# Kernel tuning notes

Hardware: AMD Instinct MI355X
Metric: run time of the kernel (lower is better)

## Reference

```python
import jax, jax.numpy as jnp
import numpy as np

B, L, D, H, NL = 4, 2048, 128, 4, 2
DH = D // H
FF = 2 * D
EPS_LN = 1e-5


def _p(key, shape, scale=0.05):
    return (jax.random.normal(key, shape, dtype=jnp.float32) * scale)


def setup_inputs() -> dict:
    key = jax.random.key(0)
    ks = jax.random.split(key, 40)
    inp = {
        "local_global": jax.random.normal(ks[0], (B, D), dtype=jnp.float32),
        "task_features": jax.random.normal(ks[1], (B, L, 15), dtype=jnp.float32),
        "privacy_features": jax.random.normal(ks[2], (B, L, 6), dtype=jnp.float32),
        "dag_features": jax.random.normal(ks[3], (B, L, 4), dtype=jnp.float32),
        # float mask in [0,1); values > 0.5 are MASKED (set to -inf) per torch code
        "attn_mask": jax.random.uniform(ks[4], (B, L, L), dtype=jnp.float32),
        # input projections (stored [in, out]; torch Linear does x @ W.T + b)
        "task_W": _p(ks[5], (15, D)), "task_b": jnp.zeros((D,), jnp.float32),
        "priv_W": _p(ks[6], (6, D)), "priv_b": jnp.zeros((D,), jnp.float32),
        "dag_W": _p(ks[7], (4, D)), "dag_b": jnp.zeros((D,), jnp.float32),
        "pre_g": jnp.ones((D,), jnp.float32), "pre_b": jnp.zeros((D,), jnp.float32),
        "post_g": jnp.ones((D,), jnp.float32), "post_b": jnp.zeros((D,), jnp.float32),
        "out_W": _p(ks[8], (D, D)), "out_b": jnp.zeros((D,), jnp.float32),
        # per-layer params stacked on leading NL axis
        "qW": _p(ks[9], (NL, D, D)), "qb": jnp.zeros((NL, D), jnp.float32),
        "kW": _p(ks[10], (NL, D, D)), "kb": jnp.zeros((NL, D), jnp.float32),
        "vW": _p(ks[11], (NL, D, D)), "vb": jnp.zeros((NL, D), jnp.float32),
        "oW": _p(ks[12], (NL, D, D)), "ob": jnp.zeros((NL, D), jnp.float32),
        "n1g": jnp.ones((NL, D), jnp.float32), "n1b": jnp.zeros((NL, D), jnp.float32),
        "n2g": jnp.ones((NL, D), jnp.float32), "n2b": jnp.zeros((NL, D), jnp.float32),
        "f1W": _p(ks[13], (NL, D, FF)), "f1b": jnp.zeros((NL, FF), jnp.float32),
        "f2W": _p(ks[14], (NL, FF, D)), "f2b": jnp.zeros((NL, D), jnp.float32),
    }
    return inp


def _layernorm(x, g, b):
    mu = x.mean(-1, keepdims=True)
    var = ((x - mu) ** 2).mean(-1, keepdims=True)
    return (x - mu) * jax.lax.rsqrt(var + EPS_LN) * g + b


def _attention(x, add_mask, Wq, bq, Wk, bk, Wv, bv, Wo, bo):
    # x: [B,L,D]; add_mask: [B,L,L] additive (0 or -inf)
    def heads(y):
        return y.reshape(B, L, H, DH).transpose(0, 2, 1, 3)  # [B,H,L,DH]
    q = heads(x @ Wq + bq)
    k = heads(x @ Wk + bk)
    v = heads(x @ Wv + bv)
    scale = 1.0 / np.sqrt(DH).astype(np.float32)
    scores = jnp.einsum('bhqd,bhkd->bhqk', q, k) * scale + add_mask[:, None]
    # fully-masked-row diagonal fixup (torch: set diag score to 0 where row max is -inf)
    row_max = scores.max(-1)                       # [B,H,L]
    fully_masked = jnp.isinf(row_max) & (row_max < 0)
    eye = jnp.eye(L, dtype=bool)
    scores = jnp.where(fully_masked[..., None] & eye, 0.0, scores)
    w = jax.nn.softmax(scores, axis=-1)
    # NaN fallback: if any NaN, replace with 1/L and renormalize (applied globally, as torch does)
    has_nan = jnp.isnan(w).any()
    fixed = jnp.nan_to_num(w, nan=1.0 / L)
    fixed = fixed / (fixed.sum(-1, keepdims=True) + 1e-8)
    w = jnp.where(has_nan, fixed, w)
    out = jnp.einsum('bhqk,bhkd->bhqd', w, v)      # [B,H,L,DH]
    out = out.transpose(0, 2, 1, 3).reshape(B, L, D)
    return out @ Wo + bo


def reference(local_global, task_features, privacy_features, dag_features, attn_mask,
              task_W, task_b, priv_W, priv_b, dag_W, dag_b,
              pre_g, pre_b, post_g, post_b, out_W, out_b,
              qW, qb, kW, kb, vW, vb, oW, ob,
              n1g, n1b, n2g, n2b, f1W, f1b, f2W, f2b):
    # normalize mask: >0.5 means masked; fix all-False rows by masking their diagonal (torch quirk)
    mb = attn_mask > 0.5                            # [B,L,L] bool, True = mask out
    need_fix = ~mb.any(-1)                          # [B,L]
    eye = jnp.eye(L, dtype=bool)
    mb = mb | (need_fix[..., None] & eye)
    add_mask = jnp.where(mb, -jnp.inf, 0.0).astype(jnp.float32)

    ctx = (task_features @ task_W + task_b) + (privacy_features @ priv_W + priv_b) \
          + (dag_features @ dag_W + dag_b)
    x = _layernorm(ctx, pre_g, pre_b)
    for i in range(NL):  # eval mode: dropout = identity
        sa = _attention(_layernorm(x, n1g[i], n1b[i]), add_mask,
                        qW[i], qb[i], kW[i], kb[i], vW[i], vb[i], oW[i], ob[i])
        x = x + sa
        h = _layernorm(x, n2g[i], n2b[i])
        ff = jax.nn.gelu(h @ f1W[i] + f1b[i], approximate=False) @ f2W[i] + f2b[i]
        x = x + ff
    enc = _layernorm(x, post_g, post_b)
    global_ctx = enc.mean(axis=1)                   # [B,D]
    fused = global_ctx + 0.1 * local_global
    aligned = fused @ out_W + out_b
    return aligned
```

## Files before the change

### kernel.cpp

```cpp
#include <hip/hip_runtime.h>
#include <hip/hip_bf16.h>

#define DEV __device__ __forceinline__

typedef float f32x4 __attribute__((ext_vector_type(4)));
typedef float f32x16 __attribute__((ext_vector_type(16)));
typedef short s16x8 __attribute__((ext_vector_type(8)));
typedef unsigned short u16x4 __attribute__((ext_vector_type(4)));
typedef __bf16 bf16x8 __attribute__((ext_vector_type(8)));

DEV bf16x8 as_bf16(s16x8 v) { return __builtin_bit_cast(bf16x8, v); }

DEV unsigned short f2bf(float f) {
    union { __hip_bfloat16 h; unsigned short u; } c;
    c.h = __float2bfloat16(f);
    return c.u;
}

DEV float bf2f(unsigned short u) {
    return __builtin_bit_cast(float, (unsigned)u << 16);
}

DEV unsigned f2bf2(float lo, float hi) {
    unsigned ulo = __builtin_bit_cast(unsigned, lo);
    unsigned uhi = __builtin_bit_cast(unsigned, hi);
    ulo = (ulo + 0x7fffu + ((ulo >> 16) & 1u)) >> 16;
    uhi = (uhi + 0x7fffu + ((uhi >> 16) & 1u)) & 0xffff0000u;
    return ulo | uhi;
}

DEV float wave_sum64(float v) {
#pragma unroll
    for (int m = 1; m < 64; m <<= 1) v += __shfl_xor(v, m, 64);
    return v;
}

DEV int rot3(int r) { return ((r << 1) | (r >> 2)) & 7; }

constexpr float QSCL = (float)(1.4426950408889634 / 5.656854249492381);

__global__ __launch_bounds__(256) void gace_setup_k(
    const float* __restrict__ am, unsigned long long* __restrict__ bits,
    const float* __restrict__ task, const float* __restrict__ priv, const float* __restrict__ dag,
    const float* __restrict__ tW, const float* __restrict__ tb,
    const float* __restrict__ pW, const float* __restrict__ pb,
    const float* __restrict__ dW, const float* __restrict__ db,
    const float* __restrict__ pre_g, const float* __restrict__ pre_b,
    float* __restrict__ x,
    const float* __restrict__ qW, const float* __restrict__ kW,
    const float* __restrict__ vW, const float* __restrict__ oW,
    const float* __restrict__ f1W, const float* __restrict__ f2W,
    const float* __restrict__ qb, const float* __restrict__ kb,
    const float* __restrict__ vb,
    unsigned short* __restrict__ wbf, float* __restrict__ bcat)
{
    __shared__ unsigned short tileS[32][33];
    const int bx = blockIdx.x;
    const int tid = threadIdx.x, wid = tid >> 6, l = tid & 63;
    if (bx < 2048) {
        const int row = bx * 4 + wid;
        const float* mrow = am + (size_t)row * 2048;
        unsigned long long myword = 0, orAll = 0, andAll = ~0ull;
#pragma unroll 4
        for (int w = 0; w < 32; ++w) {
            unsigned long long bal = __ballot(mrow[w * 64 + l] > 0.5f);
            if (w == l) myword = bal;
            orAll |= bal; andAll &= bal;
        }
        const int lrow = row & 2047;
        const int dw = lrow >> 6, dbit = lrow & 63;
        if (l == dw) {
            if (orAll == 0ull) myword |= (1ull << dbit);
            else if (andAll == ~0ull) myword &= ~(1ull << dbit);
        }
        if (l < 32) bits[(size_t)row * 32 + l] = myword;
        return;
    }
    if (bx < 4096) {
        const int row = (bx - 2048) * 4 + wid;
        const int d0 = l, d1 = l + 64;
        float a0 = tb[d0] + pb[d0] + db[d0];
        float a1 = tb[d1] + pb[d1] + db[d1];
        const float* tf = task + (size_t)row * 15;
#pragma unroll
        for (int j = 0; j < 15; ++j) { const float t = tf[j]; a0 += t * tW[j * 128 + d0]; a1 += t * tW[j * 128 + d1]; }
        const float* pf = priv + (size_t)row * 6;
#pragma unroll
        for (int j = 0; j < 6; ++j) { const float t = pf[j]; a0 += t * pW[j * 128 + d0]; a1 += t * pW[j * 128 + d1]; }
        const float* df = dag + (size_t)row * 4;
#pragma unroll
        for (int j = 0; j < 4; ++j) { const float t = df[j]; a0 += t * dW[j * 128 + d0]; a1 += t * dW[j * 128 + d1]; }
        const float s = wave_sum64(a0 + a1);
        const float mean = s * (1.f / 128.f);
        const float e0 = a0 - mean, e1 = a1 - mean;
        const float s2 = wave_sum64(e0 * e0 + e1 * e1);
        const float rs = rsqrtf(s2 * (1.f / 128.f) + 1e-5f);
        x[(size_t)row * 128 + d0] = e0 * rs * pre_g[d0] + pre_b[d0];
        x[(size_t)row * 128 + d1] = e1 * rs * pre_g[d1] + pre_b[d1];
        return;
    }
    if (bx < 4352) {
        const int t = bx - 4096;
        const int i = t >> 7, tl = t & 127;
        const float* src; int K_, N_, off, kt, nt; float scl = 1.0f;
        if (tl < 64) {
            const int y = tl >> 4, sub = tl & 15;
            kt = sub >> 2; nt = sub & 3;
            K_ = 128; N_ = 128;
            switch (y) {
                case 0:  src = qW; off = 0;     scl = QSCL; break;
                case 1:  src = kW; off = 16384; break;
                case 2:  src = vW; off = 32768; break;
                default: src = oW; off = 49152; break;
            }
        } else if (tl < 96) {
            const int sub = tl - 64; kt = sub >> 3; nt = sub & 7;
            K_ = 128; N_ = 256; src = f1W; off = 65536;
        } else {
            const int sub = tl - 96; kt = sub >> 2; nt = sub & 3;
            K_ = 256; N_ = 128; src = f2W; off = 98304;
        }
        const int per = K_ * N_;
        const int k0 = kt * 32, n0 = nt * 32;
        const int rr = tid >> 5, cc = tid & 31;
#pragma unroll
        for (int it = 0; it < 4; ++it) {
            const int r = it * 8 + rr;
            tileS[r][cc] = f2bf(src[(size_t)i * per + (size_t)(k0 + r) * N_ + n0 + cc] * scl);
        }
        __syncthreads();
#pragma unroll
        for (int it = 0; it < 4; ++it) {
            const int n = it * 8 + rr;
            wbf[(size_t)i * 131072 + off + (size_t)(n0 + n) * K_ + k0 + cc] = tileS[cc][n];
        }
        return;
    }
    for (int j = tid; j < 768; j += 256) {
        const int i = j / 384, jj = j % 384;
        float v;
        if (jj < 128)      v = qb[i * 128 + jj] * QSCL;
        else if (jj < 256) v = kb[i * 128 + jj - 128];
        else               v = vb[i * 128 + jj - 256];
        bcat[j] = v;
    }
}

__global__ __launch_bounds__(256) void gace_qkv_k(
    const float* __restrict__ xin,
    const float* __restrict__ gam, const float* __restrict__ bet,
    const unsigned short* __restrict__ Wt,
    const float* __restrict__ bias,
    unsigned short* __restrict__ qk, unsigned short* __restrict__ vtbuf)
{
    const int tid = threadIdx.x;
    const int wid = tid >> 6, l = tid & 63;
    const int g = (l >> 4) & 3, c16 = l & 15;
    const int m0 = blockIdx.x * 64 + wid * 16;
    const int n0 = blockIdx.y * 64;
    const int arow = m0 + c16;

    float v[4][8];
#pragma unroll
    for (int kc = 0; kc < 4; ++kc) {
        const f32x4 a0 = *(const f32x4*)&xin[(size_t)arow * 128 + kc * 32 + 8 * g];
        const f32x4 a1 = *(const f32x4*)&xin[(size_t)arow * 128 + kc * 32 + 8 * g + 4];
#pragma unroll
        for (int e = 0; e < 4; ++e) { v[kc][e] = a0[e]; v[kc][4 + e] = a1[e]; }
    }
    float s = 0.f;
#pragma unroll
    for (int kc = 0; kc < 4; ++kc)
#pragma unroll
        for (int e = 0; e < 8; ++e) s += v[kc][e];
    s += __shfl_xor(s, 16, 64); s += __shfl_xor(s, 32, 64);
    const float mean = s * (1.f / 128.f);
    float s2 = 0.f;
#pragma unroll
    for (int kc = 0; kc < 4; ++kc)
#pragma unroll
        for (int e = 0; e < 8; ++e) { const float d = v[kc][e] - mean; s2 += d * d; }
    s2 += __shfl_xor(s2, 16, 64); s2 += __shfl_xor(s2, 32, 64);
    const float rs = rsqrtf(s2 * (1.f / 128.f) + 1e-5f);
    s16x8 af[4];
#pragma unroll
    for (int kc = 0; kc < 4; ++kc) {
        union { s16x8 v8; unsigned d[4]; } pk;
#pragma unroll
        for (int j = 0; j < 4; ++j) {
            const int col = kc * 32 + 8 * g + 2 * j;
            const float x0 = (v[kc][2 * j] - mean) * rs * gam[col] + bet[col];
            const float x1 = (v[kc][2 * j + 1] - mean) * rs * gam[col + 1] + bet[col + 1];
            pk.d[j] = f2bf2(x0, x1);
        }
        af[kc] = pk.v8;
    }

    f32x4 acc[4];
#pragma unroll
    for (int i = 0; i < 4; ++i) acc[i] = f32x4{0.f, 0.f, 0.f, 0.f};
#pragma unroll
    for (int ns = 0; ns < 4; ++ns) {
        const unsigned short* wrow = Wt + (size_t)(n0 + 16 * ns + c16) * 128;
#pragma unroll
        for (int kc = 0; kc < 4; ++kc) {
            const s16x8 bfv = *(const s16x8*)&wrow[kc * 32 + 8 * g];
            acc[ns] = __builtin_amdgcn_mfma_f32_16x16x32_bf16(
                as_bf16(af[kc]), as_bf16(bfv), acc[ns], 0, 0, 0);
        }
    }
    if (n0 >= 256) {
        const int row0 = m0 + 4 * g;
#pragma unroll
        for (int ns = 0; ns < 4; ++ns) {
            const int n = n0 + ns * 16 + c16;
            const float bv = bias[n];
            u16x4 pk;
#pragma unroll
            for (int r = 0; r < 4; ++r) pk[r] = f2bf(acc[ns][r] + bv);
            *(u16x4*)&vtbuf[(size_t)(n - 256) * 8192 + row0] = pk;
        }
        return;
    }
#pragma unroll
    for (int ns = 0; ns < 4; ++ns) {
        const int n = n0 + ns * 16 + c16;
        const float bv = bias[n];
#pragma unroll
        for (int r = 0; r < 4; ++r)
            qk[(size_t)(m0 + 4 * g + r) * 256 + n] = f2bf(acc[ns][r] + bv);
    }
}

__global__ __launch_bounds__(512) void gace_flash8_k(
    const unsigned short* __restrict__ QK,
    const unsigned short* __restrict__ Vt,
    const unsigned long long* __restrict__ bits,
    unsigned short* __restrict__ Opb, float* __restrict__ ml)
{
    __shared__ __align__(16) unsigned short Ks[2 * 2 * 2560];
    __shared__ __align__(16) char VtB[2 * 2 * 4096];

    const int tid = threadIdx.x;
    const int wid = tid >> 6, l = tid & 63;
    const int c32 = l & 31, hi = l >> 5;
    const int bid = (blockIdx.x & 7) * 128 + (blockIdx.x >> 3);
    const int split = bid & 7, qc = (bid >> 3) & 7, h = (bid >> 6) & 3, b = bid >> 8;
    const size_t base = (size_t)b * 2048;
    const int qb0 = qc * 256 + wid * 32;
    const int q = qb0 + c32;

    const unsigned short* qrow = &QK[(base + q) * 256 + h * 32];
    const s16x8 qf0 = *(const s16x8*)&qrow[8 * hi];
    const s16x8 qf1 = *(const s16x8*)&qrow[16 + 8 * hi];
    const int rot3c = rot3(c32 & 7);

    f32x16 oacc;
#pragma unroll
    for (int i = 0; i < 16; ++i) oacc[i] = 0.f;
    float l_ = 0.f;

    const int st = tid & 255;
    const int sr = st >> 2;
    const int se = (tid & 3) << 3;
    const int lowr = sr & 31, t12 = lowr & 12;
    const int prow = (sr & 32) | (((t12 == 4) | (t12 == 8)) ? (lowr ^ 12) : lowr);
    const int rv = st >> 3;
    const int sv = tid & 7;
    const int vds = rv * 128 + 16 * (sv ^ rot3(rv & 7));

    const int kv0 = split * 256;
    const unsigned long long* bq = &bits[(base + q) * 32 + split * 4];
    const unsigned short* kgb = &QK[base * 256 + 128 + h * 32 + se];
    const unsigned short* vgb = &Vt[(size_t)(h * 32 + rv) * 8192 + base + kv0 + sv * 8];

    s16x8 kregA, kregB, vregA, vregB;
    auto LOAD = [&](int it2) {
        if (tid < 256) {
            const int kv = kv0 + it2 * 128;
            kregA = *(const s16x8*)&kgb[(size_t)(kv + sr) * 256];
            kregB = *(const s16x8*)&kgb[(size_t)(kv + 64 + sr) * 256];
        } else {
            vregA = *(const s16x8*)&vgb[it2 * 128];
            vregB = *(const s16x8*)&vgb[it2 * 128 + 64];
        }
    };
    auto STAGE = [&](int pb) {
        if (tid < 256) {
            *(s16x8*)&Ks[(pb * 2 + 0) * 2560 + prow * 40 + se] = kregA;
            *(s16x8*)&Ks[(pb * 2 + 1) * 2560 + prow * 40 + se] = kregB;
        } else {
            *(s16x8*)&VtB[(pb * 2 + 0) * 4096 + vds] = vregA;
            *(s16x8*)&VtB[(pb * 2 + 1) * 4096 + vds] = vregB;
        }
    };
    auto COMPUTE = [&](int pb, int sub, unsigned long long wb) {
        const unsigned short* KsS = &Ks[(pb * 2 + sub) * 2560];
        const char* VtS = &VtB[(pb * 2 + sub) * 4096];
        const unsigned long long wbs = wb >> (8 * hi);
        const unsigned wlo = (unsigned)wbs, whiw = (unsigned)(wbs >> 32);
        __builtin_amdgcn_s_setprio(1);
#pragma unroll
        for (int H = 0; H < 2; ++H) {
            const unsigned short* kr = &KsS[(32 * H + c32) * 40 + 8 * hi];
            f32x16 zv;
#pragma unroll
            for (int i = 0; i < 16; ++i) zv[i] = 0.f;
            f32x16 sac = __builtin_amdgcn_mfma_f32_32x32x16_bf16(
                as_bf16(*(const s16x8*)&kr[0]), as_bf16(qf0), zv, 0, 0, 0);
            sac = __builtin_amdgcn_mfma_f32_32x32x16_bf16(
                as_bf16(*(const s16x8*)&kr[16]), as_bf16(qf1), sac, 0, 0, 0);
            const unsigned word = (H == 0) ? wlo : whiw;
#pragma unroll
            for (int ch = 0; ch < 2; ++ch) {
                const int c = 2 * H + ch;
                const int bb = ch * 16;
                float p[8];
#pragma unroll
                for (int e = 0; e < 8; ++e) {
                    const float pe = exp2f(sac[ch * 8 + e]);
                    p[e] = ((word >> (bb + e)) & 1u) ? 0.f : pe;
                }
                l_ += ((p[0] + p[1]) + (p[2] + p[3])) + ((p[4] + p[5]) + (p[6] + p[7]));
                union { s16x8 v; unsigned d[4]; } pa;
#pragma unroll
                for (int j = 0; j < 4; ++j)
                    asm("v_cvt_pk_bf16_f32 %0, %1, %2"
                        : "=v"(pa.d[j]) : "v"(p[2 * j]), "v"(p[2 * j + 1]));
                const s16x8 vf = *(const s16x8*)&VtS[c32 * 128 + 16 * ((2 * c + hi) ^ rot3c)];
                oacc = __builtin_amdgcn_mfma_f32_32x32x16_bf16(
                    as_bf16(pa.v), as_bf16(vf), oacc, 0, 0, 0);
            }
        }
        __builtin_amdgcn_s_setprio(0);
    };

    unsigned long long wbv[4];
#pragma unroll
    for (int w = 0; w < 4; ++w) wbv[w] = bq[w];
    LOAD(0);
    STAGE(0);
    LOAD(1);
    __syncthreads();

#pragma unroll
    for (int it = 0; it < 2; ++it) {
        const int p = it & 1;
        COMPUTE(p, 0, wbv[2 * it]);
        if (it < 1) STAGE(p ^ 1);
        COMPUTE(p, 1, wbv[2 * it + 1]);
        if (it < 1) __syncthreads();
    }

    l_ += __shfl_xor(l_, 32, 64);
    unsigned short* orow = &Opb[((size_t)split * 8192 + base + qb0) * 128 + h * 32 + c32];
#pragma unroll
    for (int r = 0; r < 16; ++r) {
        const int qoff = (r & 3) + 8 * (r >> 2) + 4 * hi;
        orow[(size_t)qoff * 128] = f2bf(oacc[r]);
    }
    if (l < 32) ml[((size_t)split * 8192 + base + q) * 4 + h] = l_;
}

template<int QKV, int LAST>
__global__ __launch_bounds__(256) void gace_post2_k(
    const unsigned short* __restrict__ Opb, const float* __restrict__ ml,
    const unsigned short* __restrict__ oWt, const float* __restrict__ obv,
    float* __restrict__ x,
    const float* __restrict__ n2g, const float* __restrict__ n2b,
    const unsigned short* __restrict__ f1Wt, const float* __restrict__ f1b,
    const unsigned short* __restrict__ f2Wt, const float* __restrict__ f2b,
    const float* __restrict__ n1g2, const float* __restrict__ n1b2,
    const unsigned short* __restrict__ w2, const float* __restrict__ bcat2,
    unsigned short* __restrict__ qk, unsigned short* __restrict__ vtbuf,
    const float* __restrict__ post_g, const float* __restrict__ post_b,
    float* __restrict__ partial)
{
    __shared__ __align__(16) float xbuf[16][132];
    __shared__ __align__(16) unsigned short g1buf[16][264];
    __shared__ float stats[16][2];
    const int tid = threadIdx.x, wid = tid >> 6, l = tid & 63;
    const int g = (l >> 4) & 3, c16 = l & 15;
    const int m0 = blockIdx.x * 16;
    const int arow = m0 + c16;

    s16x8 af[4];
#pragma unroll
    for (int kc = 0; kc < 4; ++kc) {
        float o[8];
#pragma unroll
        for (int e = 0; e < 8; ++e) o[e] = 0.f;
        float Ls = 0.f;
#pragma unroll
        for (int sp = 0; sp < 8; ++sp) {
            const size_t ro = (size_t)sp * 8192 + arow;
            union { s16x8 v; unsigned short u[8]; } ov;
            ov.v = *(const s16x8*)&Opb[ro * 128 + kc * 32 + 8 * g];
#pragma unroll
            for (int e = 0; e < 8; ++e) o[e] += bf2f(ov.u[e]);
            Ls += ml[ro * 4 + kc];
        }
        const float inv = 1.f / Ls;
        union { s16x8 v8; unsigned d[4]; } pk;
#pragma unroll
        for (int j = 0; j < 4; ++j) pk.d[j] = f2bf2(o[2 * j] * inv, o[2 * j + 1] * inv);
        af[kc] = pk.v8;
    }
    {
        f32x4 acc2[2];
#pragma unroll
        for (int z = 0; z < 2; ++z) acc2[z] = f32x4{0.f, 0.f, 0.f, 0.f};
#pragma unroll
        for (int nsl = 0; nsl < 2; ++nsl) {
            const int ns = wid * 2 + nsl;
            const unsigned short* wrow = oWt + (size_t)(16 * ns + c16) * 128;
#pragma unroll
            for (int kc = 0; kc < 4; ++kc)
                acc2[nsl] = __builtin_amdgcn_mfma_f32_16x16x32_bf16(
                    as_bf16(af[kc]), as_bf16(*(const s16x8*)&wrow[kc * 32 + 8 * g]),
                    acc2[nsl], 0, 0, 0);
        }
#pragma unroll
        for (int nsl = 0; nsl < 2; ++nsl) {
            const int n = 16 * (wid * 2 + nsl) + c16;
            const float bv = obv[n];
#pragma unroll
            for (int r = 0; r < 4; ++r) {
                const int lr = 4 * g + r;
                xbuf[lr][n] = acc2[nsl][r] + bv + x[(size_t)(m0 + lr) * 128 + n];
            }
        }
    }
    __syncthreads();
    s16x8 af1[4];
    {
        float v2[4][8];
#pragma unroll
        for (int kc = 0; kc < 4; ++kc) {
            const f32x4 a0 = *(const f32x4*)&xbuf[c16][kc * 32 + 8 * g];
            const f32x4 a1 = *(const f32x4*)&xbuf[c16][kc * 32 + 8 * g + 4];
#pragma unroll
            for (int e = 0; e < 4; ++e) { v2[kc][e] = a0[e]; v2[kc][4 + e] = a1[e]; }
        }
        float s = 0.f;
#pragma unroll
        for (int kc = 0; kc < 4; ++kc)
#pragma unroll
            for (int e = 0; e < 8; ++e) s += v2[kc][e];
        s += __shfl_xor(s, 16, 64); s += __shfl_xor(s, 32, 64);
        const float mean = s * (1.f / 128.f);
        float s2 = 0.f;
#pragma unroll
        for (int kc = 0; kc < 4; ++kc)
#pragma unroll
            for (int e = 0; e < 8; ++e) { const float d = v2[kc][e] - mean; s2 += d * d; }
        s2 += __shfl_xor(s2, 16, 64); s2 += __shfl_xor(s2, 32, 64);
        const float rs = rsqrtf(s2 * (1.f / 128.f) + 1e-5f);
#pragma unroll
        for (int kc = 0; kc < 4; ++kc) {
            union { s16x8 v8; unsigned d[4]; } pk;
#pragma unroll
            for (int j = 0; j < 4; ++j) {
                const int col = kc * 32 + 8 * g + 2 * j;
                const float x0 = (v2[kc][2 * j] - mean) * rs * n2g[col] + n2b[col];
                const float x1 = (v2[kc][2 * j + 1] - mean) * rs * n2g[col + 1] + n2b[col + 1];
                pk.d[j] = f2bf2(x0, x1);
            }
            af1[kc] = pk.v8;
        }
    }
    {
        f32x4 accf[4];
#pragma unroll
        for (int z = 0; z < 4; ++z) accf[z] = f32x4{0.f, 0.f, 0.f, 0.f};
#pragma unroll
        for (int nsl = 0; nsl < 4; ++nsl) {
            const int ns = wid * 4 + nsl;
            const unsigned short* wrow = f1Wt + (size_t)(16 * ns + c16) * 128;
#pragma unroll
            for (int kc = 0; kc < 4; ++kc)
                accf[nsl] = __builtin_amdgcn_mfma_f32_16x16x32_bf16(
                    as_bf16(af1[kc]), as_bf16(*(const s16x8*)&wrow[kc * 32 + 8 * g]),
                    accf[nsl], 0, 0, 0);
        }
#pragma unroll
        for (int nsl = 0; nsl < 4; ++nsl) {
            const int n = 16 * (wid * 4 + nsl) + c16;
            const float bv = f1b[n];
#pragma unroll
            for (int r = 0; r < 4; ++r) {
                float vv = accf[nsl][r] + bv;
                vv = vv * 0.5f * (1.0f + erff(vv * 0.70710678118654752f));
                g1buf[4 * g + r][n] = f2bf(vv);
            }
        }
    }
    __syncthreads();
    float fx[2][4];
    {
        s16x8 af2[8];
#pragma unroll
        for (int kc = 0; kc < 8; ++kc)
            af2[kc] = *(const s16x8*)&g1buf[c16][kc * 32 + 8 * g];
        f32x4 acc2[2];
#pragma unroll
        for (int z = 0; z < 2; ++z) acc2[z] = f32x4{0.f, 0.f, 0.f, 0.f};
#pragma unroll
        for (int nsl = 0; nsl < 2; ++nsl) {
            const int ns = wid * 2 + nsl;
            const unsigned short* wrow = f2Wt + (size_t)(16 * ns + c16) * 256;
#pragma unroll
            for (int kc = 0; kc < 8; ++kc)
                acc2[nsl] = __builtin_amdgcn_mfma_f32_16x16x32_bf16(
                    as_bf16(af2[kc]), as_bf16(*(const s16x8*)&wrow[kc * 32 + 8 * g]),
                    acc2[nsl], 0, 0, 0);
        }
#pragma unroll
        for (int nsl = 0; nsl < 2; ++nsl) {
            const int n = 16 * (wid * 2 + nsl) + c16;
            const float bv = f2b[n];
#pragma unroll
            for (int r = 0; r < 4; ++r)
                fx[nsl][r] = acc2[nsl][r] + bv + xbuf[4 * g + r][n];
        }
    }
    if (!QKV && !LAST) {
#pragma unroll
        for (int nsl = 0; nsl < 2; ++nsl) {
            const int n = 16 * (wid * 2 + nsl) + c16;
#pragma unroll
            for (int r = 0; r < 4; ++r)
                x[(size_t)(m0 + 4 * g + r) * 128 + n] = fx[nsl][r];
        }
        return;
    }
#pragma unroll
    for (int nsl = 0; nsl < 2; ++nsl) {
        const int n = 16 * (wid * 2 + nsl) + c16;
#pragma unroll
        for (int r = 0; r < 4; ++r) {
            const int lr = 4 * g + r;
            if (QKV) x[(size_t)(m0 + lr) * 128 + n] = fx[nsl][r];
            xbuf[lr][n] = fx[nsl][r];
        }
    }
    __syncthreads();
    if (QKV) {
        s16x8 afq[4];
        {
            float v1[4][8];
#pragma unroll
            for (int kc = 0; kc < 4; ++kc) {
                const f32x4 a0 = *(const f32x4*)&xbuf[c16][kc * 32 + 8 * g];
                const f32x4 a1 = *(const f32x4*)&xbuf[c16][kc * 32 + 8 * g + 4];
#pragma unroll
                for (int e = 0; e < 4; ++e) { v1[kc][e] = a0[e]; v1[kc][4 + e] = a1[e]; }
            }
            float s1 = 0.f;
#pragma unroll
            for (int kc = 0; kc < 4; ++kc)
#pragma unroll
                for (int e = 0; e < 8; ++e) s1 += v1[kc][e];
            s1 += __shfl_xor(s1, 16, 64); s1 += __shfl_xor(s1, 32, 64);
            const float mean1 = s1 * (1.f / 128.f);
            float sq1 = 0.f;
#pragma unroll
            for (int kc = 0; kc < 4; ++kc)
#pragma unroll
                for (int e = 0; e < 8; ++e) { const float d = v1[kc][e] - mean1; sq1 += d * d; }
            sq1 += __shfl_xor(sq1, 16, 64); sq1 += __shfl_xor(sq1, 32, 64);
            const float rs1 = rsqrtf(sq1 * (1.f / 128.f) + 1e-5f);
#pragma unroll
            for (int kc = 0; kc < 4; ++kc) {
                union { s16x8 v8; unsigned d[4]; } pk;
#pragma unroll
                for (int j = 0; j < 4; ++j) {
                    const int col = kc * 32 + 8 * g + 2 * j;
                    const float x0 = (v1[kc][2 * j] - mean1) * rs1 * n1g2[col] + n1b2[col];
                    const float x1 = (v1[kc][2 * j + 1] - mean1) * rs1 * n1g2[col + 1] + n1b2[col + 1];
                    pk.d[j] = f2bf2(x0, x1);
                }
                afq[kc] = pk.v8;
            }
        }
#pragma unroll
        for (int j = 0; j < 6; ++j) {
            const int ns = wid * 6 + j;
            const unsigned short* wrow = w2 + (size_t)(ns * 16 + c16) * 128;
            f32x4 acc = f32x4{0.f, 0.f, 0.f, 0.f};
#pragma unroll
            for (int kc = 0; kc < 4; ++kc)
                acc = __builtin_amdgcn_mfma_f32_16x16x32_bf16(
                    as_bf16(afq[kc]), as_bf16(*(const s16x8*)&wrow[kc * 32 + 8 * g]),
                    acc, 0, 0, 0);
            const int n = ns * 16 + c16;
            const float bv = bcat2[n];
            if (ns >= 16) {
                const int row0 = m0 + 4 * g;
                u16x4 pk;
#pragma unroll
                for (int r = 0; r < 4; ++r) pk[r] = f2bf(acc[r] + bv);
                *(u16x4*)&vtbuf[(size_t)(n - 256) * 8192 + row0] = pk;
            } else {
#pragma unroll
                for (int r = 0; r < 4; ++r)
                    qk[(size_t)(m0 + 4 * g + r) * 256 + n] = f2bf(acc[r] + bv);
            }
        }
        return;
    }
    if (LAST) {
#pragma unroll
        for (int rr = 0; rr < 4; ++rr) {
            const int row = wid * 4 + rr;
            const float v0 = xbuf[row][l], v1 = xbuf[row][l + 64];
            const float s = wave_sum64(v0 + v1);
            const float mean = s * (1.f / 128.f);
            const float d0 = v0 - mean, d1 = v1 - mean;
            const float s2 = wave_sum64(d0 * d0 + d1 * d1);
            const float rstd = rsqrtf(s2 * (1.f / 128.f) + 1e-5f);
            if (l == 0) { stats[row][0] = mean; stats[row][1] = rstd; }
        }
        __syncthreads();
#pragma unroll
        for (int nsl = 0; nsl < 2; ++nsl) {
            const int ns = wid * 2 + nsl;
            const int n = 16 * ns + c16;
            const float pg = post_g[n], pb_ = post_b[n];
            float cs = 0.f;
#pragma unroll
            for (int r = 0; r < 4; ++r) {
                const int row = 4 * g + r;
                cs += (xbuf[row][n] - stats[row][0]) * stats[row][1] * pg + pb_;
            }
            cs += __shfl_xor(cs, 16, 64);
            cs += __shfl_xor(cs, 32, 64);
            if (l < 16) partial[(size_t)blockIdx.x * 128 + n] = cs;
        }
    }
}

__global__ __launch_bounds__(128) void gace_tailB_k(
    const float* __restrict__ partial, const float* __restrict__ lg,
    const float* __restrict__ oW, const float* __restrict__ obv,
    float* __restrict__ out)
{
    const int tid = threadIdx.x, b2 = blockIdx.x;
    __shared__ float fused[128];
    float s = 0.f;
#pragma unroll 8
    for (int c = 0; c < 128; ++c) s += partial[(size_t)(b2 * 128 + c) * 128 + tid];
    fused[tid] = s * (1.f / 2048.f) + 0.1f * lg[b2 * 128 + tid];
    __syncthreads();
    float r = obv[tid];
#pragma unroll 8
    for (int d2 = 0; d2 < 128; ++d2) r += fused[d2] * oW[d2 * 128 + tid];
    out[b2 * 128 + tid] = r;
}

extern "C" void kernel_launch(void* const* d_in, const int* in_sizes, int n_in,
                              void* d_out, int out_size, void* d_ws, size_t ws_size,
                              hipStream_t stream)
{
    (void)in_sizes; (void)n_in; (void)out_size; (void)ws_size;
    const float* local_global = (const float*)d_in[0];
    const float* task   = (const float*)d_in[1];
    const float* priv   = (const float*)d_in[2];
    const float* dag    = (const float*)d_in[3];
    const float* amask  = (const float*)d_in[4];
    const float* task_W = (const float*)d_in[5];
    const float* task_b = (const float*)d_in[6];
    const float* priv_W = (const float*)d_in[7];
    const float* priv_b = (const float*)d_in[8];
    const float* dag_W  = (const float*)d_in[9];
    const float* dag_b  = (const float*)d_in[10];
    const float* pre_g  = (const float*)d_in[11];
    const float* pre_b  = (const float*)d_in[12];
    const float* post_g = (const float*)d_in[13];
    const float* post_b = (const float*)d_in[14];
    const float* out_W  = (const float*)d_in[15];
    const float* out_b  = (const float*)d_in[16];
    const float* qW = (const float*)d_in[17];
    const float* qb = (const float*)d_in[18];
    const float* kW = (const float*)d_in[19];
    const float* kb = (const float*)d_in[20];
    const float* vW = (const float*)d_in[21];
    const float* vb = (const float*)d_in[22];
    const float* oW = (const float*)d_in[23];
    const float* ob = (const float*)d_in[24];
    const float* n1g = (const float*)d_in[25];
    const float* n1b = (const float*)d_in[26];
    const float* n2g = (const float*)d_in[27];
    const float* n2b = (const float*)d_in[28];
    const float* f1W = (const float*)d_in[29];
    const float* f1b = (const float*)d_in[30];
    const float* f2W = (const float*)d_in[31];
    const float* f2b = (const float*)d_in[32];

    char* ws = (char*)d_ws;
    size_t off = 0;
    auto carve = [&](size_t sz) {
        void* p = ws + off;
        off += (sz + 255) & ~(size_t)255;
        return p;
    };
    unsigned long long* bits = (unsigned long long*)carve(8192ull * 32 * 8);
    float*          x    = (float*)carve(8192ull * 128 * 4);
    unsigned short* qk   = (unsigned short*)carve(8192ull * 256 * 2);
    unsigned short* vt   = (unsigned short*)carve(128ull * 8192 * 2);
    float*          part = (float*)carve(512ull * 128 * 4);
    unsigned short* Opb  = (unsigned short*)carve(8ull * 8192 * 128 * 2);
    float*          mlb  = (float*)carve(8ull * 8192 * 4 * 4);
    unsigned short* wbf  = (unsigned short*)carve(2ull * 131072 * 2);
    float*          bcat = (float*)carve(2ull * 384 * 4);

    gace_setup_k<<<4353, 256, 0, stream>>>(
        amask, bits,
        task, priv, dag, task_W, task_b, priv_W, priv_b, dag_W, dag_b,
        pre_g, pre_b, x,
        qW, kW, vW, oW, f1W, f2W, qb, kb, vb, wbf, bcat);
    gace_qkv_k<<<dim3(128, 6), 256, 0, stream>>>(
        x, n1g, n1b, wbf, bcat, qk, vt);
    gace_flash8_k<<<1024, 512, 0, stream>>>(qk, vt, bits, Opb, mlb);
    gace_post2_k<1, 0><<<512, 256, 0, stream>>>(
        Opb, mlb, wbf + 49152, ob, x, n2g, n2b,
        wbf + 65536, f1b, wbf + 98304, f2b,
        n1g + 128, n1b + 128, wbf + 131072, bcat + 384, qk, vt,
        nullptr, nullptr, nullptr);
    gace_flash8_k<<<1024, 512, 0, stream>>>(qk, vt, bits, Opb, mlb);
    gace_post2_k<0, 1><<<512, 256, 0, stream>>>(
        Opb, mlb, wbf + 131072 + 49152, ob + 128, x, n2g + 128, n2b + 128,
        wbf + 131072 + 65536, f1b + 256, wbf + 131072 + 98304, f2b + 128,
        nullptr, nullptr, nullptr, nullptr, nullptr, nullptr,
        post_g, post_b, part);
    gace_tailB_k<<<4, 128, 0, stream>>>(part, local_global, out_W, out_b, (float*)d_out);
}
```

Measured before the change: 157.4 us.

## Split flash attention KV range into 16 chunks instead of 8

Doubles the number of KV splits in the flash attention kernel, so each block handles 128 keys instead of 256. The in-block double-buffered load/stage pipeline is replaced with a single load, sync and compute. The grid doubles to 2048 blocks, and shared memory per block is halved, which should raise occupancy and parallelism. The cost is twice as much partial output and denominator traffic, and a 16-way reduction in the post kernel.

```diff
diff --git a/kernel.cpp b/kernel.cpp
--- a/kernel.cpp
+++ b/kernel.cpp
@@ -232,20 +232,20 @@
     }
 }
 
-__global__ __launch_bounds__(512) void gace_flash8_k(
+__global__ __launch_bounds__(512) void gace_flash9_k(
     const unsigned short* __restrict__ QK,
     const unsigned short* __restrict__ Vt,
     const unsigned long long* __restrict__ bits,
     unsigned short* __restrict__ Opb, float* __restrict__ ml)
 {
-    __shared__ __align__(16) unsigned short Ks[2 * 2 * 2560];
-    __shared__ __align__(16) char VtB[2 * 2 * 4096];
+    __shared__ __align__(16) unsigned short Ks[2 * 2560];
+    __shared__ __align__(16) char VtB[2 * 4096];
 
     const int tid = threadIdx.x;
     const int wid = tid >> 6, l = tid & 63;
     const int c32 = l & 31, hi = l >> 5;
-    const int bid = (blockIdx.x & 7) * 128 + (blockIdx.x >> 3);
-    const int split = bid & 7, qc = (bid >> 3) & 7, h = (bid >> 6) & 3, b = bid >> 8;
+    const int bid = (blockIdx.x & 7) * 256 + (blockIdx.x >> 3);
+    const int split = bid & 15, qc = (bid >> 4) & 7, h = (bid >> 7) & 3, b = bid >> 9;
     const size_t base = (size_t)b * 2048;
     const int qb0 = qc * 256 + wid * 32;
     const int q = qb0 + c32;
@@ -269,34 +269,28 @@
     const int sv = tid & 7;
     const int vds = rv * 128 + 16 * (sv ^ rot3(rv & 7));
 
-    const int kv0 = split * 256;
-    const unsigned long long* bq = &bits[(base + q) * 32 + split * 4];
-    const unsigned short* kgb = &QK[base * 256 + 128 + h * 32 + se];
-    const unsigned short* vgb = &Vt[(size_t)(h * 32 + rv) * 8192 + base + kv0 + sv * 8];
-
-    s16x8 kregA, kregB, vregA, vregB;
-    auto LOAD = [&](int it2) {
-        if (tid < 256) {
-            const int kv = kv0 + it2 * 128;
-            kregA = *(const s16x8*)&kgb[(size_t)(kv + sr) * 256];
-            kregB = *(const s16x8*)&kgb[(size_t)(kv + 64 + sr) * 256];
-        } else {
-            vregA = *(const s16x8*)&vgb[it2 * 128];
-            vregB = *(const s16x8*)&vgb[it2 * 128 + 64];
-        }
-    };
-    auto STAGE = [&](int pb) {
-        if (tid < 256) {
-            *(s16x8*)&Ks[(pb * 2 + 0) * 2560 + prow * 40 + se] = kregA;
-            *(s16x8*)&Ks[(pb * 2 + 1) * 2560 + prow * 40 + se] = kregB;
-        } else {
-            *(s16x8*)&VtB[(pb * 2 + 0) * 4096 + vds] = vregA;
-            *(s16x8*)&VtB[(pb * 2 + 1) * 4096 + vds] = vregB;
-        }
-    };
-    auto COMPUTE = [&](int pb, int sub, unsigned long long wb) {
-        const unsigned short* KsS = &Ks[(pb * 2 + sub) * 2560];
-        const char* VtS = &VtB[(pb * 2 + sub) * 4096];
+    const int kv0 = split * 128;
+    const unsigned long long* bq = &bits[(base + q) * 32 + split * 2];
+    const unsigned long long wb0 = bq[0], wb1 = bq[1];
+
+    if (tid < 256) {
+        const unsigned short* kgb = &QK[base * 256 + 128 + h * 32 + se];
+        const s16x8 kregA = *(const s16x8*)&kgb[(size_t)(kv0 + sr) * 256];
+        const s16x8 kregB = *(const s16x8*)&kgb[(size_t)(kv0 + 64 + sr) * 256];
+        *(s16x8*)&Ks[0 * 2560 + prow * 40 + se] = kregA;
+        *(s16x8*)&Ks[1 * 2560 + prow * 40 + se] = kregB;
+    } else {
+        const unsigned short* vgb = &Vt[(size_t)(h * 32 + rv) * 8192 + base + kv0 + sv * 8];
+        const s16x8 vregA = *(const s16x8*)&vgb[0];
+        const s16x8 vregB = *(const s16x8*)&vgb[64];
+        *(s16x8*)&VtB[0 * 4096 + vds] = vregA;
+        *(s16x8*)&VtB[1 * 4096 + vds] = vregB;
+    }
+    __syncthreads();
+
+    auto COMPUTE = [&](int sub, unsigned long long wb) {
+        const unsigned short* KsS = &Ks[sub * 2560];
+        const char* VtS = &VtB[sub * 4096];
         const unsigned long long wbs = wb >> (8 * hi);
         const unsigned wlo = (unsigned)wbs, whiw = (unsigned)(wbs >> 32);
         __builtin_amdgcn_s_setprio(1);
@@ -335,22 +329,8 @@
         __builtin_amdgcn_s_setprio(0);
     };
 
-    unsigned long long wbv[4];
-#pragma unroll
-    for (int w = 0; w < 4; ++w) wbv[w] = bq[w];
-    LOAD(0);
-    STAGE(0);
-    LOAD(1);
-    __syncthreads();
-
-#pragma unroll
-    for (int it = 0; it < 2; ++it) {
-        const int p = it & 1;
-        COMPUTE(p, 0, wbv[2 * it]);
-        if (it < 1) STAGE(p ^ 1);
-        COMPUTE(p, 1, wbv[2 * it + 1]);
-        if (it < 1) __syncthreads();
-    }
+    COMPUTE(0, wb0);
+    COMPUTE(1, wb1);
 
     l_ += __shfl_xor(l_, 32, 64);
     unsigned short* orow = &Opb[((size_t)split * 8192 + base + qb0) * 128 + h * 32 + c32];
@@ -392,7 +372,7 @@
         for (int e = 0; e < 8; ++e) o[e] = 0.f;
         float Ls = 0.f;
 #pragma unroll
-        for (int sp = 0; sp < 8; ++sp) {
+        for (int sp = 0; sp < 16; ++sp) {
             const size_t ro = (size_t)sp * 8192 + arow;
             union { s16x8 v; unsigned short u[8]; } ov;
             ov.v = *(const s16x8*)&Opb[ro * 128 + kc * 32 + 8 * g];
@@ -709,8 +689,8 @@
     unsigned short* qk   = (unsigned short*)carve(8192ull * 256 * 2);
     unsigned short* vt   = (unsigned short*)carve(128ull * 8192 * 2);
     float*          part = (float*)carve(512ull * 128 * 4);
-    unsigned short* Opb  = (unsigned short*)carve(8ull * 8192 * 128 * 2);
-    float*          mlb  = (float*)carve(8ull * 8192 * 4 * 4);
+    unsigned short* Opb  = (unsigned short*)carve(16ull * 8192 * 128 * 2);
+    float*          mlb  = (float*)carve(16ull * 8192 * 4 * 4);
     unsigned short* wbf  = (unsigned short*)carve(2ull * 131072 * 2);
     float*          bcat = (float*)carve(2ull * 384 * 4);
 
@@ -721,13 +701,13 @@
         qW, kW, vW, oW, f1W, f2W, qb, kb, vb, wbf, bcat);
     gace_qkv_k<<<dim3(128, 6), 256, 0, stream>>>(
         x, n1g, n1b, wbf, bcat, qk, vt);
-    gace_flash8_k<<<1024, 512, 0, stream>>>(qk, vt, bits, Opb, mlb);
+    gace_flash9_k<<<2048, 512, 0, stream>>>(qk, vt, bits, Opb, mlb);
     gace_post2_k<1, 0><<<512, 256, 0, stream>>>(
         Opb, mlb, wbf + 49152, ob, x, n2g, n2b,
         wbf + 65536, f1b, wbf + 98304, f2b,
         n1g + 128, n1b + 128, wbf + 131072, bcat + 384, qk, vt,
         nullptr, nullptr, nullptr);
-    gace_flash8_k<<<1024, 512, 0, stream>>>(qk, vt, bits, Opb, mlb);
+    gace_flash9_k<<<2048, 512, 0, stream>>>(qk, vt, bits, Opb, mlb);
     gace_post2_k<0, 1><<<512, 256, 0, stream>>>(
         Opb, mlb, wbf + 131072 + 49152, ob + 128, x, n2g + 128, n2b + 128,
         wbf + 131072 + 65536, f1b + 256, wbf + 131072 + 98304, f2b + 128,
```

After: 181.6 us. 1.15x slower.
